# Performance work log

Hardware: AMD Instinct MI355X
Metric: run time of the kernel (lower is better)

Reference implementation:

```python
import jax, jax.numpy as jnp
import numpy as np

NUM_TREES = 4096
TOTAL_NODES = 1048576
D = 256


def _make_tree_sizes():
    # ragged, strictly positive sizes summing exactly to TOTAL_NODES
    rng = np.random.default_rng(0)
    cuts = np.sort(rng.choice(TOTAL_NODES - 1, NUM_TREES - 1, replace=False) + 1)
    bounds = np.concatenate([[0], cuts, [TOTAL_NODES]])
    return jnp.asarray(np.diff(bounds), dtype=jnp.int64)


def setup_inputs() -> dict:
    key = jax.random.key(0)
    embeddings = jax.random.normal(key, (TOTAL_NODES, D), dtype=jnp.float32)
    tree_sizes = _make_tree_sizes()
    return {"embeddings": embeddings, "tree_sizes": tree_sizes}


def reference(embeddings, tree_sizes):
    num_trees = tree_sizes.shape[0]
    total = embeddings.shape[0]
    # groups[j] = tree index of node j (contiguous segments)
    groups = jnp.repeat(jnp.arange(num_trees, dtype=jnp.int32), tree_sizes,
                        total_repeat_length=total)
    # segmented max over dim 0 -> [num_trees, D]
    return jax.ops.segment_max(embeddings, groups, num_segments=num_trees)
```

## Files before the change

### kernel.cpp

```cpp
#include <hip/hip_runtime.h>
#include <math.h>

#define NUM_TREES 4096
#define TOTAL_NODES 1048576
#define DCOL 256
#define DPW 64
#define SLICE 128
#define NWAVES 8192

static __device__ __forceinline__ float4 f4max(float4 a, float4 b) {
    float4 r;
    r.x = fmaxf(a.x, b.x);
    r.y = fmaxf(a.y, b.y);
    r.z = fmaxf(a.z, b.z);
    r.w = fmaxf(a.w, b.w);
    return r;
}

static __device__ __forceinline__ void atomicFmax(float* addr, float val) {
    unsigned* u = (unsigned*)addr;
    unsigned old = *u;
    while (__uint_as_float(old) < val) {
        unsigned assumed = old;
        old = atomicCAS(u, assumed, __float_as_uint(val));
        if (old == assumed) break;
    }
}

__global__ void TreeAgg_prep_init(const void* __restrict__ sizes_raw,
                                  int* __restrict__ row_off,
                                  float* __restrict__ out) {
    if (blockIdx.x == 0) {
        __shared__ int s_row[256];
        __shared__ int s_is64;
        const int t = threadIdx.x;
        const int base = t * 16;
        const int* s32 = (const int*)sizes_raw;

        int ls[16];
        int rsum = 0;
        #pragma unroll
        for (int i = 0; i < 16; ++i) { ls[i] = s32[base + i]; rsum += ls[i]; }
        s_row[t] = rsum;
        __syncthreads();
        if (t == 0) {
            long long tot = 0;
            for (int i = 0; i < 256; ++i) tot += (long long)s_row[i];
            s_is64 = (tot != (long long)TOTAL_NODES) ? 1 : 0;
        }
        __syncthreads();
        if (s_is64) {
            const long long* s64 = (const long long*)sizes_raw;
            #pragma unroll
            for (int i = 0; i < 16; ++i) ls[i] = (int)s64[base + i];
            int rs = 0;
            #pragma unroll
            for (int i = 0; i < 16; ++i) rs += ls[i];
            s_row[t] = rs;
            __syncthreads();
        }
        if (t == 0) {
            int ra = 0;
            for (int i = 0; i < 256; ++i) { int r = s_row[i]; s_row[i] = ra; ra += r; }
            row_off[NUM_TREES] = ra;
        }
        __syncthreads();
        int ro = s_row[t];
        #pragma unroll
        for (int i = 0; i < 16; ++i) { row_off[base + i] = ro; ro += ls[i]; }
    } else {
        const int i = (blockIdx.x - 1) * blockDim.x + threadIdx.x;
        const float NEG = -INFINITY;
        ((float4*)out)[i] = make_float4(NEG, NEG, NEG, NEG);
    }
}

__global__ __launch_bounds__(256, 8)
void TreeAgg_main(const float* __restrict__ emb,
                  const int* __restrict__ row_off,
                  float* __restrict__ out) {
    const int wid  = (blockIdx.x * blockDim.x + threadIdx.x) >> 6;
    const int lane = threadIdx.x & 63;

    int a = wid * SLICE;
    const int bend = a + SLICE;

    int lo = 0, hi = NUM_TREES;
    while (hi - lo > 1) {
        int mid = (lo + hi) >> 1;
        if (row_off[mid] <= a) lo = mid; else hi = mid;
    }
    int t = lo;

    const float4* __restrict__ src = (const float4*)emb;
    const float NEG = -INFINITY;
    long idx = (long)a * DPW + lane;

    while (a < bend) {
        int b = min(bend, row_off[t + 1]);
        if (b <= a) break;
        float4 acc = make_float4(NEG, NEG, NEG, NEG);
        int r = a;
        for (; r + 4 <= b; r += 4, idx += 4 * DPW) {
            float4 x = src[idx];
            float4 y = src[idx + DPW];
            float4 z = src[idx + 2 * DPW];
            float4 w = src[idx + 3 * DPW];
            acc = f4max(acc, f4max(f4max(x, y), f4max(z, w)));
        }
        for (; r < b; ++r, idx += DPW) {
            acc = f4max(acc, src[idx]);
        }
        float* dst = out + (long)t * DCOL + lane * 4;
        atomicFmax(dst + 0, acc.x);
        atomicFmax(dst + 1, acc.y);
        atomicFmax(dst + 2, acc.z);
        atomicFmax(dst + 3, acc.w);
        a = b;
        ++t;
    }
}

extern "C" void kernel_launch(void* const* d_in, const int* in_sizes, int n_in,
                              void* d_out, int out_size, void* d_ws, size_t ws_size,
                              hipStream_t stream) {
    const float* emb   = (const float*)d_in[0];
    const void*  sizes = d_in[1];
    float*       out   = (float*)d_out;

    int* row_off = (int*)d_ws;

    TreeAgg_prep_init<<<1025, 256, 0, stream>>>(sizes, row_off, out);

    TreeAgg_main<<<NWAVES * 64 / 256, 256, 0, stream>>>(emb, row_off, out);
}
```

Before: 238.7 us.

## Interleave 16-row runs across waves with integer atomicMax and non-temporal loads

Splits the node rows into small 16-row runs assigned round-robin across 4096 waves. Each run is loaded with 16 independent non-temporal loads and reduced as a tree. The CAS-loop float max is replaced by a single integer atomicMax on an order-preserving encoding, which needs an extra decode kernel at the end. Row offsets are cached in shared memory for the binary search. The cost is one more launch, more atomics per tree (one commit per run instead of per slice), and a 16KB shared-memory load per block.

After: 294.8 us. 1.24x slower.

```diff
diff --git a/kernel.cpp b/kernel.cpp
--- a/kernel.cpp
+++ b/kernel.cpp
@@ -5,11 +5,31 @@
 #define TOTAL_NODES 1048576
 #define DCOL 256
 #define DPW 64
-#define SLICE 128
-#define NWAVES 8192
+#define RUN 16
+#define NWAVES 4096
+#define NRUNS (TOTAL_NODES / RUN)
+#define SWEEPS (NRUNS / NWAVES)
 
-static __device__ __forceinline__ float4 f4max(float4 a, float4 b) {
-    float4 r;
+typedef float f4v __attribute__((ext_vector_type(4)));
+
+#if __has_builtin(__builtin_nontemporal_load)
+#define NTLOAD(p) __builtin_nontemporal_load(p)
+#else
+#define NTLOAD(p) (*(p))
+#endif
+
+static __device__ __forceinline__ unsigned enc(float f) {
+    unsigned b = __float_as_uint(f);
+    return (b & 0x80000000u) ? ~b : (b | 0x80000000u);
+}
+static __device__ __forceinline__ float dec(unsigned u) {
+    return (u & 0x80000000u) ? __uint_as_float(u ^ 0x80000000u)
+                             : __uint_as_float(~u);
+}
+#define ENC_NEG_INF 0x007FFFFFu
+
+static __device__ __forceinline__ f4v vmax4(f4v a, f4v b) {
+    f4v r;
     r.x = fmaxf(a.x, b.x);
     r.y = fmaxf(a.y, b.y);
     r.z = fmaxf(a.z, b.z);
@@ -17,19 +37,18 @@
     return r;
 }
 
-static __device__ __forceinline__ void atomicFmax(float* addr, float val) {
-    unsigned* u = (unsigned*)addr;
-    unsigned old = *u;
-    while (__uint_as_float(old) < val) {
-        unsigned assumed = old;
-        old = atomicCAS(u, assumed, __float_as_uint(val));
-        if (old == assumed) break;
-    }
+static __device__ __forceinline__ void commit(unsigned* __restrict__ out_u,
+                                              int t, int lane, f4v acc) {
+    unsigned* dst = out_u + (long)t * DCOL + lane * 4;
+    atomicMax(dst + 0, enc(acc.x));
+    atomicMax(dst + 1, enc(acc.y));
+    atomicMax(dst + 2, enc(acc.z));
+    atomicMax(dst + 3, enc(acc.w));
 }
 
 __global__ void TreeAgg_prep_init(const void* __restrict__ sizes_raw,
                                   int* __restrict__ row_off,
-                                  float* __restrict__ out) {
+                                  unsigned* __restrict__ out_u) {
     if (blockIdx.x == 0) {
         __shared__ int s_row[256];
         __shared__ int s_is64;
@@ -70,55 +89,70 @@
         for (int i = 0; i < 16; ++i) { row_off[base + i] = ro; ro += ls[i]; }
     } else {
         const int i = (blockIdx.x - 1) * blockDim.x + threadIdx.x;
-        const float NEG = -INFINITY;
-        ((float4*)out)[i] = make_float4(NEG, NEG, NEG, NEG);
+        ((uint4*)out_u)[i] = make_uint4(ENC_NEG_INF, ENC_NEG_INF, ENC_NEG_INF, ENC_NEG_INF);
     }
 }
 
-__global__ __launch_bounds__(256, 8)
+__global__ __launch_bounds__(256, 4)
 void TreeAgg_main(const float* __restrict__ emb,
                   const int* __restrict__ row_off,
-                  float* __restrict__ out) {
-    const int wid  = (blockIdx.x * blockDim.x + threadIdx.x) >> 6;
-    const int lane = threadIdx.x & 63;
+                  unsigned* __restrict__ out_u) {
+    __shared__ int s_off[NUM_TREES + 1];
+    const int tid = threadIdx.x;
+    #pragma unroll
+    for (int i = 0; i < 16; ++i) s_off[tid * 16 + i] = row_off[tid * 16 + i];
+    if (tid == 0) s_off[NUM_TREES] = row_off[NUM_TREES];
+    __syncthreads();
 
-    int a = wid * SLICE;
-    const int bend = a + SLICE;
+    const int wid  = (blockIdx.x * 256 + tid) >> 6;
+    const int lane = tid & 63;
+    const f4v* __restrict__ src = (const f4v*)emb;
+    const float NEG = -INFINITY;
 
-    int lo = 0, hi = NUM_TREES;
-    while (hi - lo > 1) {
-        int mid = (lo + hi) >> 1;
-        if (row_off[mid] <= a) lo = mid; else hi = mid;
+    for (int g = 0; g < SWEEPS; ++g) {
+        const int j = g * NWAVES + wid;
+        const int a = j * RUN;
+        const int b = a + RUN;
+
+        int lo = 0, hi = NUM_TREES;
+        while (hi - lo > 1) {
+            int mid = (lo + hi) >> 1;
+            if (s_off[mid] <= a) lo = mid; else hi = mid;
+        }
+        int t = lo;
+
+        if (s_off[t + 1] >= b) {
+            const long ib = (long)a * DPW + lane;
+            f4v v[RUN];
+            #pragma unroll
+            for (int k = 0; k < RUN; ++k) v[k] = NTLOAD(src + ib + (long)k * DPW);
+            #pragma unroll
+            for (int s = RUN / 2; s > 0; s >>= 1)
+                #pragma unroll
+                for (int k = 0; k < s; ++k) v[k] = vmax4(v[k], v[k + s]);
+            commit(out_u, t, lane, v[0]);
+        } else {
+            int aa = a;
+            while (aa < b) {
+                const int ee = min(b, s_off[t + 1]);
+                f4v acc = { NEG, NEG, NEG, NEG };
+                long idx = (long)aa * DPW + lane;
+                for (int r = aa; r < ee; ++r, idx += DPW)
+                    acc = vmax4(acc, NTLOAD(src + idx));
+                commit(out_u, t, lane, acc);
+                aa = ee;
+                if (aa < b) ++t;
+            }
+        }
     }
-    int t = lo;
+}
 
-    const float4* __restrict__ src = (const float4*)emb;
-    const float NEG = -INFINITY;
-    long idx = (long)a * DPW + lane;
-
-    while (a < bend) {
-        int b = min(bend, row_off[t + 1]);
-        if (b <= a) break;
-        float4 acc = make_float4(NEG, NEG, NEG, NEG);
-        int r = a;
-        for (; r + 4 <= b; r += 4, idx += 4 * DPW) {
-            float4 x = src[idx];
-            float4 y = src[idx + DPW];
-            float4 z = src[idx + 2 * DPW];
-            float4 w = src[idx + 3 * DPW];
-            acc = f4max(acc, f4max(f4max(x, y), f4max(z, w)));
-        }
-        for (; r < b; ++r, idx += DPW) {
-            acc = f4max(acc, src[idx]);
-        }
-        float* dst = out + (long)t * DCOL + lane * 4;
-        atomicFmax(dst + 0, acc.x);
-        atomicFmax(dst + 1, acc.y);
-        atomicFmax(dst + 2, acc.z);
-        atomicFmax(dst + 3, acc.w);
-        a = b;
-        ++t;
-    }
+__global__ void TreeAgg_decode(unsigned* __restrict__ out_u) {
+    const int i = blockIdx.x * blockDim.x + threadIdx.x;
+    uint4 v = ((uint4*)out_u)[i];
+    float4 f;
+    f.x = dec(v.x); f.y = dec(v.y); f.z = dec(v.z); f.w = dec(v.w);
+    ((float4*)out_u)[i] = f;
 }
 
 extern "C" void kernel_launch(void* const* d_in, const int* in_sizes, int n_in,
@@ -126,11 +160,13 @@
                               hipStream_t stream) {
     const float* emb   = (const float*)d_in[0];
     const void*  sizes = d_in[1];
-    float*       out   = (float*)d_out;
+    unsigned*    out_u = (unsigned*)d_out;
 
     int* row_off = (int*)d_ws;
 
-    TreeAgg_prep_init<<<1025, 256, 0, stream>>>(sizes, row_off, out);
+    TreeAgg_prep_init<<<1025, 256, 0, stream>>>(sizes, row_off, out_u);
 
-    TreeAgg_main<<<NWAVES * 64 / 256, 256, 0, stream>>>(emb, row_off, out);
+    TreeAgg_main<<<NWAVES * 64 / 256, 256, 0, stream>>>(emb, row_off, out_u);
+
+    TreeAgg_decode<<<1024, 256, 0, stream>>>(out_u);
 }
```
